# Kernel tuning notes

Measured on AMD Instinct MI355X. Metric: run time of the kernel, lower is better.

## Reference

```python
import jax, jax.numpy as jnp
import numpy as np

NUM_EMBEDDING = 8192
EMBEDDING_DIM = 512
BS = 16384
NEG_SLOPE = 0.01  # torch LeakyReLU default


def setup_inputs() -> dict:
    key = jax.random.key(0)
    k1, k2, k3, k4, k5, k6, k7 = jax.random.split(key, 7)
    d, K = EMBEDDING_DIM, NUM_EMBEDDING
    s1 = 1.0 / np.sqrt(d)
    return {
        "encoded_eeg": jax.random.normal(k1, (BS, d), dtype=jnp.float32),
        "encoded_mel": jax.random.normal(k2, (BS, d), dtype=jnp.float32),
        "embeddings": jax.random.normal(k3, (K, d), dtype=jnp.float32),
        "W1": jax.random.uniform(k4, (d, d), jnp.float32, -s1, s1),
        "b1": jax.random.uniform(k5, (d,), jnp.float32, -s1, s1),
        "W2": jax.random.uniform(k6, (K, d), jnp.float32, -s1, s1),
        "b2": jax.random.uniform(k7, (K,), jnp.float32, -s1, s1),
    }


def reference(encoded_eeg, encoded_mel, embeddings, W1, b1, W2, b2):
    # --- nearest-codebook indices for mel (detached in original) ---
    flat_mel = encoded_mel.reshape(-1, EMBEDDING_DIM)
    dists = (jnp.sum(embeddings ** 2, axis=1)[None, :]
             + jnp.sum(flat_mel ** 2, axis=1, keepdims=True)
             - 2.0 * flat_mel @ embeddings.T)  # [BS, K]
    mel_indices = jnp.argmin(dists, axis=-1)  # [BS]

    # --- small MLP logits over eeg ---
    flat_eeg = encoded_eeg.reshape(-1, EMBEDDING_DIM)
    h = flat_eeg @ W1.T + b1
    h = jnp.where(h >= 0, h, NEG_SLOPE * h)  # LeakyReLU
    logits = h @ W2.T + b2  # [BS, K]

    eeg_indices = jnp.argmax(logits, axis=-1)
    acc_rate = jnp.mean((eeg_indices == mel_indices).astype(jnp.float32))

    # cross entropy (mean over batch)
    logp = jax.nn.log_softmax(logits, axis=-1)
    loss = -jnp.mean(jnp.take_along_axis(logp, mel_indices[:, None], axis=1))
    return (loss, acc_rate)
```

## Files before the change

kernel.cpp:

```cpp
#include <hip/hip_runtime.h>
#include <hip/hip_bf16.h>
#include <hip/hip_fp8.h>

#define BSZ 16384
#define DIM 512
#define NEMB 8192
#define NEG 0.01f
#define NSPLIT 8
#define NG 64

typedef __attribute__((ext_vector_type(8))) short short8;
typedef __attribute__((ext_vector_type(4))) float f32x4;
typedef __attribute__((ext_vector_type(2))) long long2v;
typedef __attribute__((ext_vector_type(4))) int i32x4;
typedef __attribute__((ext_vector_type(8))) int i32x8;

typedef const __attribute__((address_space(1))) void GVT;
typedef __attribute__((address_space(3))) void LVT;

__device__ __forceinline__ void gl_lds16(const void* g, void* l) {
    __builtin_amdgcn_global_load_lds((GVT*)g, (LVT*)l, 16, 0, 0);
}

__device__ __forceinline__ float bf2f(unsigned short u) {
    union { unsigned int i; float f; } c; c.i = ((unsigned int)u) << 16; return c.f;
}
__device__ __forceinline__ unsigned short f2bf(float f) {
    union { __hip_bfloat16 h; unsigned short u; } c; c.h = __float2bfloat16(f); return c.u;
}
__device__ __forceinline__ unsigned char f2fp8(float f) {
    __hip_fp8_e4m3 t(f); return (unsigned char)t.__x;
}
__device__ __forceinline__ unsigned int fkey(float f) {
    unsigned int u = __float_as_uint(f);
    return u ^ ((unsigned int)((int)u >> 31) | 0x80000000u);
}

__device__ __forceinline__ size_t pack_addr(int r, int k) {
    int kg = k >> 6, ko = k & 63;
    int half = ko >> 5, lq = (ko & 31) >> 3, sub = ko & 7;
    int L = lq * 16 + (r & 15);
    return ((size_t)((r >> 4) * 8 + kg) << 10) + (size_t)(L << 4) + (half << 3) + sub;
}

__device__ __forceinline__ void pipe_barrier8() {
    asm volatile("s_waitcnt vmcnt(8) lgkmcnt(0)\ns_barrier" ::: "memory");
}
__device__ __forceinline__ void plain_barrier() {
    asm volatile("s_barrier" ::: "memory");
}

#define ISSUE8(G, BUF) do { \
    int Gm = (G) & (NG - 1); \
    size_t off = (size_t)((Gm & 7) << 10); \
    size_t bo  = off + ((size_t)(Gm >> 3) << 16); \
    gl_lds16(gA8 + off,         &sA8[BUF][uWd]); \
    gl_lds16(gA8 + off + 32768, &sA8[BUF][uWd + 4096]); \
    gl_lds16(gB8 + bo,          &sB8[BUF][uWd]); \
    gl_lds16(gB8 + bo + 32768,  &sB8[BUF][uWd + 4096]); \
} while (0)

#define COMPUTE16(BA, BB) do { \
    i32x8 fa[4], fb[4]; \
    _Pragma("unroll") for (int i = 0; i < 4; i++) { \
        i32x4 al = *(const i32x4*)&sA8[BA][offA[i]]; \
        i32x4 ah = *(const i32x4*)&sA8[BB][offA[i]]; \
        i32x4 bl = *(const i32x4*)&sB8[BA][offB[i]]; \
        i32x4 bh = *(const i32x4*)&sB8[BB][offB[i]]; \
        fa[i] = __builtin_shufflevector(al, ah, 0, 1, 2, 3, 4, 5, 6, 7); \
        fb[i] = __builtin_shufflevector(bl, bh, 0, 1, 2, 3, 4, 5, 6, 7); \
    } \
    _Pragma("unroll") for (int mi = 0; mi < 4; mi++) \
        _Pragma("unroll") for (int ni = 0; ni < 4; ni++) \
            acc[mi][ni] = __builtin_amdgcn_mfma_scale_f32_16x16x128_f8f6f4( \
                fa[mi], fb[ni], acc[mi][ni], 0, 0, 0, 0x7F7F7F7Fu, 0, 0x7F7F7F7Fu); \
} while (0)

__global__ void k_prep(const float* __restrict__ eeg, const float* __restrict__ mel,
                       const float* __restrict__ emb, const float* __restrict__ W2,
                       const float* __restrict__ W1,
                       unsigned short* __restrict__ o_eeg, unsigned short* __restrict__ o_w1,
                       unsigned char* __restrict__ o_mel8, unsigned char* __restrict__ o_emb8,
                       unsigned char* __restrict__ o_w28,
                       float* __restrict__ enorm,
                       float* __restrict__ acc2, int* __restrict__ cnt) {
    int bid = blockIdx.x, tid = threadIdx.x;
    if (bid == 0 && tid == 0) { acc2[0] = 0.f; acc2[1] = 0.f; *cnt = 0; }
    if (bid < 1024) {
        const int n_big = BSZ * DIM / 4;
        const int n_mid = NEMB * DIM / 4;
        const int n_w1  = DIM * DIM / 4;
        const int total = n_big * 2 + n_mid * 2 + n_w1;
        for (int i = bid * 256 + tid; i < total; i += 1024 * 256) {
            int j = i;
            if (j < n_big) {
                float4 v = ((const float4*)eeg)[j];
                ushort4 o; o.x = f2bf(v.x); o.y = f2bf(v.y); o.z = f2bf(v.z); o.w = f2bf(v.w);
                ((ushort4*)o_eeg)[j] = o;
            } else if ((j -= n_big) < n_w1) {
                float4 v = ((const float4*)W1)[j];
                ushort4 o; o.x = f2bf(v.x); o.y = f2bf(v.y); o.z = f2bf(v.z); o.w = f2bf(v.w);
                ((ushort4*)o_w1)[j] = o;
            } else if ((j -= n_w1) < n_big) {
                float4 v = ((const float4*)mel)[j];
                uchar4 o; o.x = f2fp8(v.x); o.y = f2fp8(v.y); o.z = f2fp8(v.z); o.w = f2fp8(v.w);
                *(uchar4*)(o_mel8 + pack_addr(j >> 7, (j & 127) * 4)) = o;
            } else if ((j -= n_big) < n_mid) {
                float4 v = ((const float4*)emb)[j];
                uchar4 o; o.x = f2fp8(v.x); o.y = f2fp8(v.y); o.z = f2fp8(v.z); o.w = f2fp8(v.w);
                *(uchar4*)(o_emb8 + pack_addr(j >> 7, (j & 127) * 4)) = o;
            } else {
                j -= n_mid;
                float4 v = ((const float4*)W2)[j];
                uchar4 o; o.x = f2fp8(v.x); o.y = f2fp8(v.y); o.z = f2fp8(v.z); o.w = f2fp8(v.w);
                *(uchar4*)(o_w28 + pack_addr(j >> 7, (j & 127) * 4)) = o;
            }
        }
    } else {
        int w = tid >> 6, lane = tid & 63;
        int row0 = (bid - 1024) * 8 + w * 2;
        #pragma unroll
        for (int t = 0; t < 2; t++) {
            int row = row0 + t;
            const float4* p = (const float4*)(emb + (size_t)row * DIM) + lane * 2;
            float4 a = p[0], b = p[1];
            float s = a.x*a.x + a.y*a.y + a.z*a.z + a.w*a.w
                    + b.x*b.x + b.y*b.y + b.z*b.z + b.w*b.w;
            #pragma unroll
            for (int d = 1; d < 64; d <<= 1) s += __shfl_xor(s, d);
            if (lane == 0) enorm[row] = s;
        }
    }
}

__launch_bounds__(256, 2)
__global__ void k_hgemm(const unsigned short* __restrict__ A,
                        const unsigned short* __restrict__ B,
                        const float* __restrict__ b1,
                        unsigned short* __restrict__ H,
                        unsigned char* __restrict__ H8) {
    __shared__ __align__(16) unsigned short sA[4096], sB[4096];
    int tid = threadIdx.x;
    int w = tid >> 6, lane = tid & 63;
    int wr = w >> 1, wc = w & 1;
    int lquad = lane >> 4, l15 = lane & 15;
    int mt = blockIdx.x >> 2, nt = blockIdx.x & 3;
    int m0 = mt * 128, n0 = nt * 128;

    int e0 = w * 512 + lane * 8;
    int r0 = e0 >> 5, ce = e0 & 31;
    const unsigned short* gA0 = A + (m0 + r0) * DIM + ce;
    const unsigned short* gA1 = gA0 + 64 * DIM;
    const unsigned short* gB0 = B + (n0 + r0) * DIM + ce;
    const unsigned short* gB1 = gB0 + 64 * DIM;
    unsigned short* lA0 = sA + w * 512;  unsigned short* lA1 = sA + (w + 4) * 512;
    unsigned short* lB0 = sB + w * 512;  unsigned short* lB1 = sB + (w + 4) * 512;

    int offA[4], offB[4];
    #pragma unroll
    for (int i = 0; i < 4; i++) {
        offA[i] = (wr * 64 + i * 16 + l15) * 32 + lquad * 8;
        offB[i] = (wc * 64 + i * 16 + l15) * 32 + lquad * 8;
    }

    f32x4 acc[4][4];
    #pragma unroll
    for (int mi = 0; mi < 4; mi++)
        #pragma unroll
        for (int ni = 0; ni < 4; ni++) acc[mi][ni] = 0;

    for (int kk = 0; kk < 16; kk++) {
        gl_lds16(gA0, lA0); gl_lds16(gA1, lA1);
        gl_lds16(gB0, lB0); gl_lds16(gB1, lB1);
        gA0 += 32; gA1 += 32; gB0 += 32; gB1 += 32;
        __syncthreads();
        short8 af[4], bf_[4];
        #pragma unroll
        for (int i = 0; i < 4; i++) {
            af[i]  = *(const short8*)&sA[offA[i]];
            bf_[i] = *(const short8*)&sB[offB[i]];
        }
        #pragma unroll
        for (int mi = 0; mi < 4; mi++)
            #pragma unroll
            for (int ni = 0; ni < 4; ni++)
                acc[mi][ni] = __builtin_amdgcn_mfma_f32_16x16x32_bf16(af[mi], bf_[ni], acc[mi][ni], 0, 0, 0);
        __syncthreads();
    }

    #pragma unroll
    for (int ni = 0; ni < 4; ni++) {
        int col = n0 + wc * 64 + ni * 16 + l15;
        float bv = b1[col];
        #pragma unroll
        for (int mi = 0; mi < 4; mi++) {
            int rowb = m0 + wr * 64 + mi * 16 + lquad * 4;
            #pragma unroll
            for (int rg = 0; rg < 4; rg++) {
                float v = acc[mi][ni][rg] + bv;
                v = v >= 0.f ? v : NEG * v;
                H[(rowb + rg) * DIM + col] = f2bf(v);
                H8[pack_addr(rowb + rg, col)] = f2fp8(v);
            }
        }
    }
}

__launch_bounds__(256, 2)
__global__ void k_big(const unsigned char* __restrict__ Mel8,
                      const unsigned char* __restrict__ Emb8,
                      const unsigned char* __restrict__ H8,
                      const unsigned char* __restrict__ W28,
                      const float* __restrict__ enorm,
                      const float* __restrict__ b2,
                      float* __restrict__ p_s,
                      unsigned int* __restrict__ p_pmax,
                      unsigned int* __restrict__ p_pmin) {
    __shared__ __align__(16) unsigned char sA8[4][8192], sB8[4][8192];
    __shared__ float sAux[1024];
    __shared__ float red_s[256];
    __shared__ unsigned int red_pm[256];
    int tid = threadIdx.x;
    int w = tid >> 6, lane = tid & 63;
    int wr = w >> 1, wc = w & 1;
    int lquad = lane >> 4, l15 = lane & 15;
    int bid = blockIdx.x;
    int is_logits = bid & 1;
    int id = bid >> 1;
    int mt = id >> 3, split = id & 7;
    int m0 = mt * 128, nbase = split * (NEMB / NSPLIT);

    int uWd = w * 1024;
    const unsigned char* gA8 = (is_logits ? H8 : Mel8) + (size_t)(m0 + 16 * w) * 512 + lane * 16;
    const unsigned char* gB8 = (is_logits ? W28 : Emb8) + (size_t)(nbase + 16 * w) * 512 + lane * 16;

    int offA[4], offB[4];
    #pragma unroll
    for (int i = 0; i < 4; i++) {
        offA[i] = (wr * 4 + i) * 1024 + lane * 16;
        offB[i] = (wc * 4 + i) * 1024 + lane * 16;
    }

    #pragma unroll
    for (int j = 0; j < 4; j++) {
        int c = tid + j * 256;
        sAux[c] = is_logits ? b2[nbase + c] : (enorm[nbase + c] - 512.0f);
    }

    ISSUE8(0, 0);
    ISSUE8(1, 1);
    ISSUE8(2, 2);
    ISSUE8(3, 3);

    f32x4 acc[4][4];
    #pragma unroll
    for (int mi = 0; mi < 4; mi++)
        #pragma unroll
        for (int ni = 0; ni < 4; ni++) acc[mi][ni] = 0;

    float s[16];
    unsigned int pbest[16];
    unsigned int pinit = is_logits ? 0u : 0xFFFFFFFFu;
    #pragma unroll
    for (int r = 0; r < 16; r++) { s[r] = 0.f; pbest[r] = pinit; }

    for (int g = 0; g < NG; g += 2) {
        int sa = g & 3, sb = sa + 1;
        pipe_barrier8();
        COMPUTE16(sa, sb);
        plain_barrier();
        ISSUE8(g + 4, sa);
        ISSUE8(g + 5, sb);
        if (((g + 1) & 7) == 7) {
            int c0off = ((g + 1) >> 3) << 7;
            if (is_logits) {
                #pragma unroll
                for (int ni = 0; ni < 4; ni++) {
                    int j = c0off + wc * 64 + ni * 16 + l15;
                    float bb = sAux[j];
                    unsigned int ic = (unsigned int)(NEMB - 1 - (nbase + j));
                    #pragma unroll
                    for (int mi = 0; mi < 4; mi++)
                        #pragma unroll
                        for (int rg = 0; rg < 4; rg++) {
                            float logit = acc[mi][ni][rg] + bb;
                            int r = mi * 4 + rg;
                            s[r] += __expf(logit);
                            unsigned int pk = (fkey(logit) & 0xFFFFE000u) | ic;
                            pbest[r] = pbest[r] > pk ? pbest[r] : pk;
                            acc[mi][ni][rg] = 0.f;
                        }
                }
            } else {
                #pragma unroll
                for (int ni = 0; ni < 4; ni++) {
                    int j = c0off + wc * 64 + ni * 16 + l15;
                    float en = sAux[j];
                    unsigned int cl = (unsigned int)(nbase + j);
                    #pragma unroll
                    for (int mi = 0; mi < 4; mi++)
                        #pragma unroll
                        for (int rg = 0; rg < 4; rg++) {
                            float d = fmaf(-2.f, acc[mi][ni][rg], en);
                            unsigned int pk = (fkey(d) & 0xFFFFE000u) | cl;
                            int r = mi * 4 + rg;
                            pbest[r] = pbest[r] < pk ? pbest[r] : pk;
                            acc[mi][ni][rg] = 0.f;
                        }
                }
            }
        }
    }

    if (is_logits) {
        #pragma unroll
        for (int r = 0; r < 16; r++)
            #pragma unroll
            for (int d = 1; d < 16; d <<= 1) {
                s[r] += __shfl_xor(s[r], d);
                unsigned int o = (unsigned int)__shfl_xor((int)pbest[r], d);
                pbest[r] = pbest[r] > o ? pbest[r] : o;
            }
        if (l15 == 0) {
            #pragma unroll
            for (int mi = 0; mi < 4; mi++)
                #pragma unroll
                for (int rg = 0; rg < 4; rg++) {
                    int r2 = (wr * 64 + mi * 16 + lquad * 4 + rg) * 2 + wc;
                    red_s[r2] = s[mi * 4 + rg];
                    red_pm[r2] = pbest[mi * 4 + rg];
                }
        }
        __syncthreads();
        if (tid < 128) {
            float S = red_s[2 * tid] + red_s[2 * tid + 1];
            unsigned int a = red_pm[2 * tid], b = red_pm[2 * tid + 1];
            int pidx = split * BSZ + m0 + tid;
            p_s[pidx] = S;
            p_pmax[pidx] = a > b ? a : b;
        }
    } else {
        #pragma unroll
        for (int r = 0; r < 16; r++)
            #pragma unroll
            for (int d = 1; d < 16; d <<= 1) {
                unsigned int o = (unsigned int)__shfl_xor((int)pbest[r], d);
                pbest[r] = pbest[r] < o ? pbest[r] : o;
            }
        if (l15 == 0) {
            #pragma unroll
            for (int mi = 0; mi < 4; mi++)
                #pragma unroll
                for (int rg = 0; rg < 4; rg++)
                    red_pm[(wr * 64 + mi * 16 + lquad * 4 + rg) * 2 + wc] = pbest[mi * 4 + rg];
        }
        __syncthreads();
        if (tid < 128) {
            unsigned int a = red_pm[2 * tid], b = red_pm[2 * tid + 1];
            p_pmin[split * BSZ + m0 + tid] = a < b ? a : b;
        }
    }
}

__global__ void k_tail(const float* __restrict__ p_s, const unsigned int* __restrict__ p_pmax,
                       const unsigned int* __restrict__ p_pmin,
                       const unsigned short* __restrict__ H,
                       const float* __restrict__ W2,
                       const float* __restrict__ b2,
                       float* __restrict__ acc2, int* __restrict__ cnt,
                       float* __restrict__ out) {
    __shared__ int s_idx[256];
    __shared__ float s_l1[256], s_match[256];
    __shared__ float s_d[4];
    int bid = blockIdx.x, tid = threadIdx.x;
    int w = tid >> 6, lane = tid & 63;
    int r = bid * 256 + tid;

    float S = 0.f; unsigned int PM = 0u, PN = 0xFFFFFFFFu;
    #pragma unroll
    for (int sp = 0; sp < NSPLIT; sp++) {
        S += p_s[sp * BSZ + r];
        unsigned int a = p_pmax[sp * BSZ + r];
        PM = PM > a ? PM : a;
        unsigned int b = p_pmin[sp * BSZ + r];
        PN = PN < b ? PN : b;
    }
    int eidx = (NEMB - 1) - (int)(PM & 0x1FFFu);
    int midx = (int)(PN & 0x1FFFu);
    s_idx[tid] = midx;
    s_l1[tid] = __logf(S) - b2[midx];
    s_match[tid] = (eidx == midx) ? 1.f : 0.f;
    __syncthreads();

    float d0 = 0.f, d1 = 0.f;
    for (int j = 0; j < 64; j++) {
        int rr = w * 64 + j;
        int ridx = s_idx[rr];
        uint4 hv = *(const uint4*)(H + (size_t)(bid * 256 + rr) * DIM + lane * 8);
        const float4* wp = (const float4*)(W2 + (size_t)ridx * DIM + lane * 8);
        float4 w0 = wp[0], w1 = wp[1];
        float p = bf2f((unsigned short)(hv.x & 0xffff)) * w0.x + bf2f((unsigned short)(hv.x >> 16)) * w0.y
                + bf2f((unsigned short)(hv.y & 0xffff)) * w0.z + bf2f((unsigned short)(hv.y >> 16)) * w0.w
                + bf2f((unsigned short)(hv.z & 0xffff)) * w1.x + bf2f((unsigned short)(hv.z >> 16)) * w1.y
                + bf2f((unsigned short)(hv.w & 0xffff)) * w1.z + bf2f((unsigned short)(hv.w >> 16)) * w1.w;
        if (j & 1) d1 += p; else d0 += p;
    }
    float ds = d0 + d1;
    #pragma unroll
    for (int d = 1; d < 64; d <<= 1) ds += __shfl_xor(ds, d);
    if (lane == 0) s_d[w] = ds;

    __syncthreads();
    for (int st = 128; st > 0; st >>= 1) {
        if (tid < st) { s_l1[tid] += s_l1[tid + st]; s_match[tid] += s_match[tid + st]; }
        __syncthreads();
    }
    if (tid == 0) {
        float loss_blk = s_l1[0] - (s_d[0] + s_d[1] + s_d[2] + s_d[3]);
        atomicAdd(&acc2[0], loss_blk * (1.0f / BSZ));
        atomicAdd(&acc2[1], s_match[0] * (1.0f / BSZ));
        __threadfence();
        if (atomicAdd(cnt, 1) == 63) {
            float L = atomicAdd(&acc2[0], 0.f);
            float M = atomicAdd(&acc2[1], 0.f);
            out[0] = L; out[1] = M;
        }
    }
}

extern "C" void kernel_launch(void* const* d_in, const int* in_sizes, int n_in,
                              void* d_out, int out_size, void* d_ws, size_t ws_size,
                              hipStream_t stream) {
    const float* eeg = (const float*)d_in[0];
    const float* mel = (const float*)d_in[1];
    const float* emb = (const float*)d_in[2];
    const float* W1  = (const float*)d_in[3];
    const float* b1  = (const float*)d_in[4];
    const float* W2  = (const float*)d_in[5];
    const float* b2  = (const float*)d_in[6];
    float* out = (float*)d_out;

    unsigned short* ws_eeg = (unsigned short*)d_ws;
    unsigned short* ws_w1  = ws_eeg + (size_t)BSZ * DIM;
    unsigned short* ws_h   = ws_w1  + (size_t)DIM * DIM;
    unsigned char*  ws_h8  = (unsigned char*)(ws_h + (size_t)BSZ * DIM);
    unsigned char*  ws_mel8 = ws_h8  + (size_t)BSZ * DIM;
    unsigned char*  ws_emb8 = ws_mel8 + (size_t)BSZ * DIM;
    unsigned char*  ws_w28  = ws_emb8 + (size_t)NEMB * DIM;
    float* ws_en  = (float*)(ws_w28 + (size_t)NEMB * DIM);
    float* p_s    = ws_en + NEMB;
    unsigned int* p_pmax = (unsigned int*)(p_s + (size_t)NSPLIT * BSZ);
    unsigned int* p_pmin = p_pmax + (size_t)NSPLIT * BSZ;
    float* acc2   = (float*)(p_pmin + (size_t)NSPLIT * BSZ);
    int*   cnt    = (int*)(acc2 + 2);

    k_prep<<<2048, 256, 0, stream>>>(eeg, mel, emb, W2, W1,
                                     ws_eeg, ws_w1, ws_mel8, ws_emb8, ws_w28,
                                     ws_en, acc2, cnt);
    k_hgemm<<<(BSZ / 128) * (DIM / 128), 256, 0, stream>>>(ws_eeg, ws_w1, b1, ws_h, ws_h8);
    k_big<<<(BSZ / 128) * NSPLIT * 2, 256, 0, stream>>>(ws_mel8, ws_emb8, ws_h8, ws_w28,
                                                        ws_en, b2, p_s, p_pmax, p_pmin);
    k_tail<<<BSZ / 256, 256, 0, stream>>>(p_s, p_pmax, p_pmin, ws_h, W2, b2, acc2, cnt, out);
}
```

Baseline: 360.3 us.

## Shrink k_big tile to 128x64 with 1x4 warp layout for higher occupancy

The k_big GEMM tile drops from 128x128 to 128x64 columns per pass. The K-group count doubles so each block still covers its 1024-column split. Each warp now owns 32 full rows across all 64 columns, which removes the cross-warp LDS reduction and its __syncthreads; partials are written straight from registers. Accumulators and LDS per block shrink so three blocks fit per CU, and s_setprio is raised around the MFMA burst. The trade-off is lower arithmetic intensity per byte loaded, since the A tile is reloaded twice as often.

```diff
diff --git a/kernel.cpp b/kernel.cpp
--- a/kernel.cpp
+++ b/kernel.cpp
@@ -7,7 +7,7 @@
 #define NEMB 8192
 #define NEG 0.01f
 #define NSPLIT 8
-#define NG 64
+#define NG 128
 
 typedef __attribute__((ext_vector_type(8))) short short8;
 typedef __attribute__((ext_vector_type(4))) float f32x4;
@@ -43,37 +43,40 @@
     return ((size_t)((r >> 4) * 8 + kg) << 10) + (size_t)(L << 4) + (half << 3) + sub;
 }
 
-__device__ __forceinline__ void pipe_barrier8() {
-    asm volatile("s_waitcnt vmcnt(8) lgkmcnt(0)\ns_barrier" ::: "memory");
+__device__ __forceinline__ void pipe_barrier6() {
+    asm volatile("s_waitcnt vmcnt(6) lgkmcnt(0)\ns_barrier" ::: "memory");
 }
 __device__ __forceinline__ void plain_barrier() {
     asm volatile("s_barrier" ::: "memory");
 }
 
-#define ISSUE8(G, BUF) do { \
+#define ISSUE6(G, BUF) do { \
     int Gm = (G) & (NG - 1); \
-    size_t off = (size_t)((Gm & 7) << 10); \
-    size_t bo  = off + ((size_t)(Gm >> 3) << 16); \
-    gl_lds16(gA8 + off,         &sA8[BUF][uWd]); \
-    gl_lds16(gA8 + off + 32768, &sA8[BUF][uWd + 4096]); \
-    gl_lds16(gB8 + bo,          &sB8[BUF][uWd]); \
-    gl_lds16(gB8 + bo + 32768,  &sB8[BUF][uWd + 4096]); \
+    size_t aoff = (size_t)((Gm & 7) << 10); \
+    size_t boff = aoff + ((size_t)(Gm >> 3) << 15); \
+    gl_lds16(gA8 + aoff,         &sA8[BUF][uWd]); \
+    gl_lds16(gA8 + aoff + 32768, &sA8[BUF][uWd + 4096]); \
+    gl_lds16(gB8 + boff,         &sB8[BUF][uWd]); \
 } while (0)
 
-#define COMPUTE16(BA, BB) do { \
-    i32x8 fa[4], fb[4]; \
-    _Pragma("unroll") for (int i = 0; i < 4; i++) { \
+#define COMPUTE8(BA, BB) do { \
+    i32x8 fa[2], fb[4]; \
+    _Pragma("unroll") for (int i = 0; i < 2; i++) { \
         i32x4 al = *(const i32x4*)&sA8[BA][offA[i]]; \
         i32x4 ah = *(const i32x4*)&sA8[BB][offA[i]]; \
+        fa[i] = __builtin_shufflevector(al, ah, 0, 1, 2, 3, 4, 5, 6, 7); \
+    } \
+    _Pragma("unroll") for (int i = 0; i < 4; i++) { \
         i32x4 bl = *(const i32x4*)&sB8[BA][offB[i]]; \
         i32x4 bh = *(const i32x4*)&sB8[BB][offB[i]]; \
-        fa[i] = __builtin_shufflevector(al, ah, 0, 1, 2, 3, 4, 5, 6, 7); \
         fb[i] = __builtin_shufflevector(bl, bh, 0, 1, 2, 3, 4, 5, 6, 7); \
     } \
-    _Pragma("unroll") for (int mi = 0; mi < 4; mi++) \
+    __builtin_amdgcn_s_setprio(1); \
+    _Pragma("unroll") for (int mi = 0; mi < 2; mi++) \
         _Pragma("unroll") for (int ni = 0; ni < 4; ni++) \
             acc[mi][ni] = __builtin_amdgcn_mfma_scale_f32_16x16x128_f8f6f4( \
                 fa[mi], fb[ni], acc[mi][ni], 0, 0, 0, 0x7F7F7F7Fu, 0, 0x7F7F7F7Fu); \
+    __builtin_amdgcn_s_setprio(0); \
 } while (0)
 
 __global__ void k_prep(const float* __restrict__ eeg, const float* __restrict__ mel,
@@ -206,7 +209,7 @@
     }
 }
 
-__launch_bounds__(256, 2)
+__launch_bounds__(256, 3)
 __global__ void k_big(const unsigned char* __restrict__ Mel8,
                       const unsigned char* __restrict__ Emb8,
                       const unsigned char* __restrict__ H8,
@@ -216,13 +219,10 @@
                       float* __restrict__ p_s,
                       unsigned int* __restrict__ p_pmax,
                       unsigned int* __restrict__ p_pmin) {
-    __shared__ __align__(16) unsigned char sA8[4][8192], sB8[4][8192];
+    __shared__ __align__(16) unsigned char sA8[4][8192], sB8[4][4096];
     __shared__ float sAux[1024];
-    __shared__ float red_s[256];
-    __shared__ unsigned int red_pm[256];
     int tid = threadIdx.x;
     int w = tid >> 6, lane = tid & 63;
-    int wr = w >> 1, wc = w & 1;
     int lquad = lane >> 4, l15 = lane & 15;
     int bid = blockIdx.x;
     int is_logits = bid & 1;
@@ -234,12 +234,11 @@
     const unsigned char* gA8 = (is_logits ? H8 : Mel8) + (size_t)(m0 + 16 * w) * 512 + lane * 16;
     const unsigned char* gB8 = (is_logits ? W28 : Emb8) + (size_t)(nbase + 16 * w) * 512 + lane * 16;
 
-    int offA[4], offB[4];
-    #pragma unroll
-    for (int i = 0; i < 4; i++) {
-        offA[i] = (wr * 4 + i) * 1024 + lane * 16;
-        offB[i] = (wc * 4 + i) * 1024 + lane * 16;
-    }
+    int offA[2], offB[4];
+    #pragma unroll
+    for (int i = 0; i < 2; i++) offA[i] = (w * 2 + i) * 1024 + lane * 16;
+    #pragma unroll
+    for (int i = 0; i < 4; i++) offB[i] = i * 1024 + lane * 16;
 
     #pragma unroll
     for (int j = 0; j < 4; j++) {
@@ -247,40 +246,40 @@
         sAux[c] = is_logits ? b2[nbase + c] : (enorm[nbase + c] - 512.0f);
     }
 
-    ISSUE8(0, 0);
-    ISSUE8(1, 1);
-    ISSUE8(2, 2);
-    ISSUE8(3, 3);
-
-    f32x4 acc[4][4];
-    #pragma unroll
-    for (int mi = 0; mi < 4; mi++)
+    ISSUE6(0, 0);
+    ISSUE6(1, 1);
+    ISSUE6(2, 2);
+    ISSUE6(3, 3);
+
+    f32x4 acc[2][4];
+    #pragma unroll
+    for (int mi = 0; mi < 2; mi++)
         #pragma unroll
         for (int ni = 0; ni < 4; ni++) acc[mi][ni] = 0;
 
-    float s[16];
-    unsigned int pbest[16];
+    float s[8];
+    unsigned int pbest[8];
     unsigned int pinit = is_logits ? 0u : 0xFFFFFFFFu;
     #pragma unroll
-    for (int r = 0; r < 16; r++) { s[r] = 0.f; pbest[r] = pinit; }
+    for (int r = 0; r < 8; r++) { s[r] = 0.f; pbest[r] = pinit; }
 
     for (int g = 0; g < NG; g += 2) {
         int sa = g & 3, sb = sa + 1;
-        pipe_barrier8();
-        COMPUTE16(sa, sb);
+        pipe_barrier6();
+        COMPUTE8(sa, sb);
         plain_barrier();
-        ISSUE8(g + 4, sa);
-        ISSUE8(g + 5, sb);
+        ISSUE6(g + 4, sa);
+        ISSUE6(g + 5, sb);
         if (((g + 1) & 7) == 7) {
-            int c0off = ((g + 1) >> 3) << 7;
+            int c0off = ((g + 1) >> 3) << 6;
             if (is_logits) {
                 #pragma unroll
                 for (int ni = 0; ni < 4; ni++) {
-                    int j = c0off + wc * 64 + ni * 16 + l15;
+                    int j = c0off + ni * 16 + l15;
                     float bb = sAux[j];
                     unsigned int ic = (unsigned int)(NEMB - 1 - (nbase + j));
                     #pragma unroll
-                    for (int mi = 0; mi < 4; mi++)
+                    for (int mi = 0; mi < 2; mi++)
                         #pragma unroll
                         for (int rg = 0; rg < 4; rg++) {
                             float logit = acc[mi][ni][rg] + bb;
@@ -294,11 +293,11 @@
             } else {
                 #pragma unroll
                 for (int ni = 0; ni < 4; ni++) {
-                    int j = c0off + wc * 64 + ni * 16 + l15;
+                    int j = c0off + ni * 16 + l15;
                     float en = sAux[j];
                     unsigned int cl = (unsigned int)(nbase + j);
                     #pragma unroll
-                    for (int mi = 0; mi < 4; mi++)
+                    for (int mi = 0; mi < 2; mi++)
                         #pragma unroll
                         for (int rg = 0; rg < 4; rg++) {
                             float d = fmaf(-2.f, acc[mi][ni][rg], en);
@@ -314,7 +313,7 @@
 
     if (is_logits) {
         #pragma unroll
-        for (int r = 0; r < 16; r++)
+        for (int r = 0; r < 8; r++)
             #pragma unroll
             for (int d = 1; d < 16; d <<= 1) {
                 s[r] += __shfl_xor(s[r], d);
@@ -323,25 +322,18 @@
             }
         if (l15 == 0) {
             #pragma unroll
-            for (int mi = 0; mi < 4; mi++)
+            for (int mi = 0; mi < 2; mi++)
                 #pragma unroll
                 for (int rg = 0; rg < 4; rg++) {
-                    int r2 = (wr * 64 + mi * 16 + lquad * 4 + rg) * 2 + wc;
-                    red_s[r2] = s[mi * 4 + rg];
-                    red_pm[r2] = pbest[mi * 4 + rg];
+                    int row = w * 32 + mi * 16 + lquad * 4 + rg;
+                    int pidx = split * BSZ + m0 + row;
+                    p_s[pidx] = s[mi * 4 + rg];
+                    p_pmax[pidx] = pbest[mi * 4 + rg];
                 }
         }
-        __syncthreads();
-        if (tid < 128) {
-            float S = red_s[2 * tid] + red_s[2 * tid + 1];
-            unsigned int a = red_pm[2 * tid], b = red_pm[2 * tid + 1];
-            int pidx = split * BSZ + m0 + tid;
-            p_s[pidx] = S;
-            p_pmax[pidx] = a > b ? a : b;
-        }
     } else {
         #pragma unroll
-        for (int r = 0; r < 16; r++)
+        for (int r = 0; r < 8; r++)
             #pragma unroll
             for (int d = 1; d < 16; d <<= 1) {
                 unsigned int o = (unsigned int)__shfl_xor((int)pbest[r], d);
@@ -349,15 +341,12 @@
             }
         if (l15 == 0) {
             #pragma unroll
-            for (int mi = 0; mi < 4; mi++)
+            for (int mi = 0; mi < 2; mi++)
                 #pragma unroll
-                for (int rg = 0; rg < 4; rg++)
-                    red_pm[(wr * 64 + mi * 16 + lquad * 4 + rg) * 2 + wc] = pbest[mi * 4 + rg];
-        }
-        __syncthreads();
-        if (tid < 128) {
-            unsigned int a = red_pm[2 * tid], b = red_pm[2 * tid + 1];
-            p_pmin[split * BSZ + m0 + tid] = a < b ? a : b;
+                for (int rg = 0; rg < 4; rg++) {
+                    int row = w * 32 + mi * 16 + lquad * 4 + rg;
+                    p_pmin[split * BSZ + m0 + row] = pbest[mi * 4 + rg];
+                }
         }
     }
 }
```

After: 382.4 us. 6.2% more time.
